# Optimization experiments

Measured on AMD Instinct MI355X. Metric: run time of the kernel, lower is better.

Reference implementation:

```python
import jax, jax.numpy as jnp
import numpy as np
from jax import lax

NEG = -10000.0


def setup_inputs() -> dict:
    key = jax.random.key(0)
    ks = jax.random.split(key, 16)
    T, V, E, H, NT = 2048, 50000, 512, 512, 48  # H = per-direction hidden (hidden_dim//2)
    start, end = NT - 2, NT - 1

    def rn(k, shape, scale=0.05):
        return jax.random.normal(k, shape, jnp.float32) * scale

    words = jax.random.randint(ks[0], (T,), 0, V)
    embed = rn(ks[1], (V, E), 0.1)
    Wih_f = rn(ks[2], (4 * H, E)); Whh_f = rn(ks[3], (4 * H, H))
    bih_f = rn(ks[4], (4 * H,));   bhh_f = rn(ks[5], (4 * H,))
    Wih_b = rn(ks[6], (4 * H, E)); Whh_b = rn(ks[7], (4 * H, H))
    bih_b = rn(ks[8], (4 * H,));   bhh_b = rn(ks[9], (4 * H,))
    W_out = rn(ks[10], (NT, 2 * H)); b_out = rn(ks[11], (NT,))
    transitions = jax.random.normal(ks[12], (NT, NT), jnp.float32)
    # match __init__: no transition into START, none out of END
    transitions = transitions.at[start, :].set(NEG).at[:, end].set(NEG)
    h0 = rn(ks[13], (2, H), 1.0)  # [fwd, bwd] initial hidden (torch.randn in init_hidden)
    c0 = rn(ks[14], (2, H), 1.0)
    return dict(words=words, embed=embed,
                Wih_f=Wih_f, Whh_f=Whh_f, bih_f=bih_f, bhh_f=bhh_f,
                Wih_b=Wih_b, Whh_b=Whh_b, bih_b=bih_b, bhh_b=bhh_b,
                W_out=W_out, b_out=b_out, transitions=transitions,
                h0=h0, c0=c0, start_tag=start, end_tag=end)


def _lstm_dir(x, h0, c0, Wih, Whh, bih, bhh, reverse):
    # x: [T, E]. Precompute input contribution for all steps (one big GEMM).
    xW = x @ Wih.T + (bih + bhh)  # [T, 4H]

    def step(carry, g_in):
        h, c = carry
        g = g_in + h @ Whh.T  # [4H]
        i, f, gg, o = jnp.split(g, 4)
        i = jax.nn.sigmoid(i); f = jax.nn.sigmoid(f)
        gg = jnp.tanh(gg);     o = jax.nn.sigmoid(o)
        c = f * c + i * gg
        h = o * jnp.tanh(c)
        return (h, c), h

    _, hs = lax.scan(step, (h0, c0), xW, reverse=reverse)
    return hs  # [T, H], aligned with input time order


def reference(words, embed, Wih_f, Whh_f, bih_f, bhh_f,
              Wih_b, Whh_b, bih_b, bhh_b,
              W_out, b_out, transitions, h0, c0, start_tag, end_tag):
    x = embed[words]  # [T, E]
    hf = _lstm_dir(x, h0[0], c0[0], Wih_f, Whh_f, bih_f, bhh_f, reverse=False)
    hb = _lstm_dir(x, h0[1], c0[1], Wih_b, Whh_b, bih_b, bhh_b, reverse=True)
    frames = jnp.concatenate([hf, hb], axis=-1) @ W_out.T + b_out  # [T, NT] emissions

    nt = transitions.shape[0]
    tT = transitions.T  # tT[from, to]
    alpha0 = jnp.full((nt,), NEG, frames.dtype).at[start_tag].set(0.0)

    def vstep(alpha, frame):
        # smat[i, j] = alpha[i] + frame[j] + transitions[j, i]
        smat = alpha[:, None] + frame[None, :] + tT
        return smat.max(axis=0), jnp.argmax(smat, axis=0)

    alpha, backtrace = lax.scan(vstep, alpha0, frames)  # backtrace: [T, NT]
    final = alpha + transitions[end_tag]
    best_last = jnp.argmax(final)
    score = final[best_last]

    def back(tag, bp):
        prev = bp[tag]
        return prev, prev

    _, path_head = lax.scan(back, best_last, backtrace[1:], reverse=True)  # [T-1]
    best_path = jnp.concatenate([path_head, best_last[None]])  # [T]
    return score, best_path
```

## Files before the change

kernel.cpp:

```cpp
#include <hip/hip_runtime.h>

#define TT 2048
#define HH 512
#define EE 512
#define NTAGS 48
#define G4 2048
#define NWG 16
#define CANARY 1.0e30f

#define OFF_XW    0ULL
#define OFF_HCAT  (OFF_XW   + 2ULL*TT*G4*4ULL)
#define OFF_FRM   (OFF_HCAT + (unsigned long long)TT*1024ULL*4ULL)
#define OFF_HBUF  (OFF_FRM  + (unsigned long long)TT*NTAGS*4ULL)
#define OFF_BP    (OFF_HBUF + 2ULL*4ULL*HH*4ULL)

__global__ __launch_bounds__(256) void k_xw(
    const int* __restrict__ words, const float* __restrict__ embed,
    const float* __restrict__ WihF, const float* __restrict__ WihB,
    const float* __restrict__ bihF, const float* __restrict__ bhhF,
    const float* __restrict__ bihB, const float* __restrict__ bhhB,
    float* __restrict__ xw, float* __restrict__ hbuf)
{
    const int tid = threadIdx.x;
    const int bx = blockIdx.x, by = blockIdx.y, dir = blockIdx.z;

    if (bx == 0 && by == 0) {
        for (int j = tid; j < 4*HH; j += 256)
            hbuf[dir*4*HH + j] = CANARY;
    }

    const float* Wih = dir ? WihB : WihF;
    const float* bi  = dir ? bihB : bihF;
    const float* bh  = dir ? bhhB : bhhF;

    __shared__ float sa[32][64];
    __shared__ float sb[32][64];
    __shared__ int   wds[64];
    if (tid < 64) wds[tid] = words[by*64 + tid];
    const int tx = tid & 15, ty = tid >> 4;
    float acc[4][4] = {};
    __syncthreads();

    for (int k0 = 0; k0 < EE; k0 += 32) {
        #pragma unroll
        for (int u = 0; u < 2; u++) {
            int idx = tid*2 + u;
            int row = idx >> 3, kq = idx & 7;
            float4 av = *(const float4*)&embed[(size_t)wds[row]*EE + k0 + kq*4];
            float4 bv = *(const float4*)&Wih[(size_t)(bx*64 + row)*EE + k0 + kq*4];
            sa[kq*4+0][row] = av.x; sa[kq*4+1][row] = av.y;
            sa[kq*4+2][row] = av.z; sa[kq*4+3][row] = av.w;
            sb[kq*4+0][row] = bv.x; sb[kq*4+1][row] = bv.y;
            sb[kq*4+2][row] = bv.z; sb[kq*4+3][row] = bv.w;
        }
        __syncthreads();
        #pragma unroll
        for (int k = 0; k < 32; k++) {
            float4 a = *(const float4*)&sa[k][ty*4];
            float4 b = *(const float4*)&sb[k][tx*4];
            acc[0][0] += a.x*b.x; acc[0][1] += a.x*b.y; acc[0][2] += a.x*b.z; acc[0][3] += a.x*b.w;
            acc[1][0] += a.y*b.x; acc[1][1] += a.y*b.y; acc[1][2] += a.y*b.z; acc[1][3] += a.y*b.w;
            acc[2][0] += a.z*b.x; acc[2][1] += a.z*b.y; acc[2][2] += a.z*b.z; acc[2][3] += a.z*b.w;
            acc[3][0] += a.w*b.x; acc[3][1] += a.w*b.y; acc[3][2] += a.w*b.z; acc[3][3] += a.w*b.w;
        }
        __syncthreads();
    }

    float* outp = xw + (size_t)dir*TT*G4;
    const int rbase = bx*64 + tx*4;
    float4 bi4 = *(const float4*)&bi[rbase];
    float4 bh4 = *(const float4*)&bh[rbase];
    float4 bias = make_float4(bi4.x+bh4.x, bi4.y+bh4.y, bi4.z+bh4.z, bi4.w+bh4.w);
    #pragma unroll
    for (int i = 0; i < 4; i++) {
        int t = by*64 + ty*4 + i;
        float4 v = make_float4(acc[i][0]+bias.x, acc[i][1]+bias.y,
                               acc[i][2]+bias.z, acc[i][3]+bias.w);
        *(float4*)&outp[(size_t)t*G4 + rbase] = v;
    }
}

__global__ __launch_bounds__(512, 2) void k_lstm(
    const float* __restrict__ WhhF, const float* __restrict__ WhhB,
    const float* __restrict__ h0, const float* __restrict__ c0,
    const float* __restrict__ xw,
    float* __restrict__ hbuf, float* __restrict__ hcat)
{
    const int bid = blockIdx.x;
    const int dir = bid >> 4;
    const int w   = bid & 15;
    const float* Whh = dir ? WhhB : WhhF;
    const float* xwD = xw + (size_t)dir*TT*G4;
    float* hb = hbuf + dir*4*HH;

    const int tid  = threadIdx.x;
    const int v    = tid >> 6;
    const int l    = tid & 63;
    const int hi   = l >> 4;
    const int gate = (l >> 2) & 3;
    const int q    = l & 3;
    const int hidx = w*32 + v*4 + hi;
    const int row  = gate*HH + hidx;
    const int lb   = l & ~15;

    float4 wreg[32];
    {
        const float4* wr = (const float4*)&Whh[(size_t)row*HH + q*128];
        #pragma unroll
        for (int k = 0; k < 32; k++) wreg[k] = wr[k];
        #pragma unroll
        for (int k = 0; k < 32; k++)
            asm volatile("" : "+v"(wreg[k].x), "+v"(wreg[k].y),
                              "+v"(wreg[k].z), "+v"(wreg[k].w));
    }
    float c = c0[dir*HH + hidx];

    __shared__ __align__(16) float hsh[2][2064];

    {
        float hv = h0[dir*HH + tid];
        #pragma unroll
        for (int r = 0; r < 4; r++) hsh[0][r*516 + tid] = hv;
    }
    __syncthreads();

    float xv = xwD[(size_t)(dir ? TT-1 : 0)*G4 + row];

    for (int s = 0; s < TT; s++) {
        const float* hq = &hsh[s & 1][q*644];
        float p0=0.f,p1=0.f,p2=0.f,p3=0.f;
        #pragma unroll
        for (int k = 0; k < 32; k++) {
            float4 hv = *(const float4*)&hq[4*k];
            p0 += wreg[k].x*hv.x; p1 += wreg[k].y*hv.y;
            p2 += wreg[k].z*hv.z; p3 += wreg[k].w*hv.w;
        }
        float part = (p0+p1)+(p2+p3);
        part += __shfl_xor(part, 1);
        part += __shfl_xor(part, 2);
        if (q == 0) part += xv;

        float gi = __shfl(part, lb);
        float gf = __shfl(part, lb + 4);
        float gg = __shfl(part, lb + 8);
        float go = __shfl(part, lb + 12);

        float i_ = 1.f/(1.f + __expf(-gi) * 0.f + expf(-gi));
        i_ = 1.f/(1.f + expf(-gi));
        float f_ = 1.f/(1.f + expf(-gf));
        float g_ = tanhf(gg);
        float o_ = 1.f/(1.f + expf(-go));
        c = f_*c + i_*g_;
        float hn = o_*tanhf(c);

        const int time = dir ? (TT-1-s) : s;
        if ((l & 15) == 0) {
            hcat[(size_t)time*1024 + dir*HH + hidx] = hn;
            if (s+1 < TT) {
                __hip_atomic_store(&hb[((s+1)&3)*HH + hidx], hn,
                                   __ATOMIC_RELAXED, __HIP_MEMORY_SCOPE_AGENT);
                __hip_atomic_store(&hb[((s+3)&3)*HH + hidx], CANARY,
                                   __ATOMIC_RELAXED, __HIP_MEMORY_SCOPE_AGENT);
            }
        }

        if (s+1 < TT) {
            asm volatile("s_waitcnt vmcnt(0)" ::: "memory");

            xv = xwD[(size_t)(dir ? TT-2-s : s+1)*G4 + row];

            const float* addr = &hb[((s+1)&3)*HH + tid];
            float hv;
            for (;;) {
                hv = __hip_atomic_load(addr, __ATOMIC_RELAXED,
                                       __HIP_MEMORY_SCOPE_AGENT);
                if (hv != CANARY) break;
                __builtin_amdgcn_s_sleep(2);
            }
            #pragma unroll
            for (int r = 0; r < 4; r++) hsh[(s+1)&1][r*516 + tid] = hv;
            __syncthreads();
        }
    }
}

__global__ __launch_bounds__(64) void k_frames(
    const float* __restrict__ hcat, const float* __restrict__ Wout,
    const float* __restrict__ bout, float* __restrict__ frames)
{
    const int t = blockIdx.x, tid = threadIdx.x;
    __shared__ float hrow[1024];
    const float4* src  = (const float4*)&hcat[(size_t)t*1024];
    float4* dst4 = (float4*)hrow;
    #pragma unroll
    for (int u = 0; u < 4; u++) dst4[u*64 + tid] = src[u*64 + tid];
    __syncthreads();
    if (tid < NTAGS) {
        float acc = bout[tid];
        const float4* wr = (const float4*)&Wout[(size_t)tid*1024];
        #pragma unroll 16
        for (int e = 0; e < 256; e++) {
            float4 wv = wr[e];
            float4 hv = dst4[e];
            acc += wv.x*hv.x + wv.y*hv.y + wv.z*hv.z + wv.w*hv.w;
        }
        frames[t*NTAGS + tid] = acc;
    }
}

#define CH 256
__global__ __launch_bounds__(256) void k_viterbi(
    const float* __restrict__ frames, const float* __restrict__ trans,
    const int* __restrict__ startp, const int* __restrict__ endp,
    unsigned char* __restrict__ bp, float* __restrict__ out)
{
    const int tid = threadIdx.x;
    const int grp = tid / NTAGS;
    const int j   = tid % NTAGS;
    __shared__ float alpha[2][NTAGS];
    __shared__ float red[4][NTAGS];
    __shared__ int   redarg[4][NTAGS];
    __shared__ float frbuf[2][NTAGS];
    __shared__ __align__(16) unsigned char bps[CH*NTAGS];
    __shared__ int s_tag;

    float tr[12];
    if (grp < 4) {
        #pragma unroll
        for (int u = 0; u < 12; u++) tr[u] = trans[j*NTAGS + grp*12 + u];
    }
    const int start_tag = *startp;
    if (tid < NTAGS) alpha[0][tid] = (tid == start_tag) ? 0.f : -10000.f;
    const bool is_pf = (tid >= 192 && tid < 192 + NTAGS);
    if (is_pf) frbuf[0][tid-192] = frames[tid-192];
    __syncthreads();

    for (int t = 0; t < TT; t++) {
        float fpre = 0.f;
        if (is_pf && t+1 < TT) fpre = frames[(t+1)*NTAGS + (tid-192)];
        if (grp < 4) {
            float best = -3.0e38f; int barg = 0;
            #pragma unroll
            for (int u = 0; u < 12; u++) {
                float sv = alpha[t&1][grp*12+u] + tr[u];
                if (sv > best) { best = sv; barg = grp*12+u; }
            }
            red[grp][j] = best; redarg[grp][j] = barg;
        }
        __syncthreads();
        if (tid < NTAGS) {
            float b = red[0][tid]; int a = redarg[0][tid];
            #pragma unroll
            for (int g2 = 1; g2 < 4; g2++) {
                float v = red[g2][tid];
                if (v > b) { b = v; a = redarg[g2][tid]; }
            }
            bp[t*NTAGS + tid] = (unsigned char)a;
            alpha[(t+1)&1][tid] = b + frbuf[t&1][tid];
        }
        __syncthreads();
        if (is_pf && t+1 < TT) frbuf[(t+1)&1][tid-192] = fpre;
    }

    if (tid == 0) {
        const int end_tag = *endp;
        float best = -3.0e38f; int bl = 0;
        for (int j2 = 0; j2 < NTAGS; j2++) {
            float v = alpha[0][j2] + trans[end_tag*NTAGS + j2];
            if (v > best) { best = v; bl = j2; }
        }
        out[0] = best;
        out[1 + TT - 1] = (float)bl;
        s_tag = bl;
    }
    __syncthreads();

    for (int base = TT - CH; base >= 0; base -= CH) {
        {
            const float4* srcr = (const float4*)&bp[(size_t)(base + tid)*NTAGS];
            float4* dstr = (float4*)&bps[tid*NTAGS];
            dstr[0] = srcr[0]; dstr[1] = srcr[1]; dstr[2] = srcr[2];
        }
        __syncthreads();
        if (tid == 0) {
            int tag = s_tag;
            const int thi = base + CH - 1;
            const int tlo = (base == 0) ? 1 : base;
            for (int t = thi; t >= tlo; t--) {
                tag = bps[(t - base)*NTAGS + tag];
                out[t] = (float)tag;
            }
            s_tag = tag;
        }
        __syncthreads();
    }
}

extern "C" void kernel_launch(void* const* d_in, const int* in_sizes, int n_in,
                              void* d_out, int out_size, void* d_ws, size_t ws_size,
                              hipStream_t stream)
{
    const int*   words = (const int*)  d_in[0];
    const float* embed = (const float*)d_in[1];
    const float* WihF  = (const float*)d_in[2];
    const float* WhhF  = (const float*)d_in[3];
    const float* bihF  = (const float*)d_in[4];
    const float* bhhF  = (const float*)d_in[5];
    const float* WihB  = (const float*)d_in[6];
    const float* WhhB  = (const float*)d_in[7];
    const float* bihB  = (const float*)d_in[8];
    const float* bhhB  = (const float*)d_in[9];
    const float* Wout  = (const float*)d_in[10];
    const float* bout  = (const float*)d_in[11];
    const float* trans = (const float*)d_in[12];
    const float* h0    = (const float*)d_in[13];
    const float* c0    = (const float*)d_in[14];
    const int*   startp= (const int*)  d_in[15];
    const int*   endp  = (const int*)  d_in[16];

    char* ws = (char*)d_ws;
    float* xw   = (float*)(ws + OFF_XW);
    float* hcat = (float*)(ws + OFF_HCAT);
    float* frm  = (float*)(ws + OFF_FRM);
    float* hbuf = (float*)(ws + OFF_HBUF);
    unsigned char* bp = (unsigned char*)(ws + OFF_BP);

    dim3 g1(32, 32, 2);
    k_xw<<<g1, 256, 0, stream>>>(words, embed, WihF, WihB, bihF, bhhF,
                                 bihB, bhhB, xw, hbuf);
    k_lstm<<<dim3(2*NWG), 512, 0, stream>>>(WhhF, WhhB, h0, c0, xw, hbuf, hcat);
    k_frames<<<dim3(TT), 64, 0, stream>>>(hcat, Wout, bout, frm);
    k_viterbi<<<dim3(1), 256, 0, stream>>>(frm, trans, startp, endp, bp, (float*)d_out);
}
```

Measured before the change: 5.253 ms.

## Restructure LSTM recurrent matvec to split K across 16 lanes per hidden unit

Each lane now holds weights for all four gates over a 32-element slice of the hidden vector and reduces across 16 lanes with xor shuffles. Previously each lane handled one gate row over a quarter of K. The shared hidden buffer shrinks from four replicated padded copies to one padded copy. The store lane no longer polls, so a neighbouring lane loads its element, and the spin loops drop sleep and gain an iteration guard. The aim is cheaper LDS traffic and a shorter critical path per timestep, at the cost of more shuffle rounds. The guard can silently break out early and let stale canary values through.

```diff
diff --git a/kernel.cpp b/kernel.cpp
--- a/kernel.cpp
+++ b/kernel.cpp
@@ -97,88 +97,114 @@
     const int v    = tid >> 6;
     const int l    = tid & 63;
     const int hi   = l >> 4;
-    const int gate = (l >> 2) & 3;
-    const int q    = l & 3;
+    const int k16  = l & 15;
     const int hidx = w*32 + v*4 + hi;
-    const int row  = gate*HH + hidx;
-    const int lb   = l & ~15;
-
-    float4 wreg[32];
-    {
-        const float4* wr = (const float4*)&Whh[(size_t)row*HH + q*128];
-        #pragma unroll
-        for (int k = 0; k < 32; k++) wreg[k] = wr[k];
-        #pragma unroll
-        for (int k = 0; k < 32; k++)
-            asm volatile("" : "+v"(wreg[k].x), "+v"(wreg[k].y),
-                              "+v"(wreg[k].z), "+v"(wreg[k].w));
-    }
+
+    float4 wreg[4][8];
+    #pragma unroll
+    for (int g = 0; g < 4; g++) {
+        const float4* wr = (const float4*)&Whh[(size_t)(g*HH + hidx)*HH + k16*32];
+        #pragma unroll
+        for (int t = 0; t < 8; t++) wreg[g][t] = wr[t];
+    }
+    #pragma unroll
+    for (int g = 0; g < 4; g++)
+        #pragma unroll
+        for (int t = 0; t < 8; t++)
+            asm volatile("" : "+v"(wreg[g][t].x), "+v"(wreg[g][t].y),
+                              "+v"(wreg[g][t].z), "+v"(wreg[g][t].w));
+
     float c = c0[dir*HH + hidx];
 
-    __shared__ __align__(16) float hsh[2][2064];
-
-    {
-        float hv = h0[dir*HH + tid];
-        #pragma unroll
-        for (int r = 0; r < 4; r++) hsh[0][r*516 + tid] = hv;
-    }
-    __syncthreads();
-
-    float xv = xwD[(size_t)(dir ? TT-1 : 0)*G4 + row];
+    __shared__ __align__(16) float hsh[2][16*36];
+
+    hsh[0][(tid>>5)*36 + (tid&31)] = h0[dir*HH + tid];
+    __syncthreads();
+
+    float xv = 0.f;
+    if (k16 < 4) xv = xwD[(size_t)(dir ? TT-1 : 0)*G4 + k16*HH + hidx];
 
     for (int s = 0; s < TT; s++) {
-        const float* hq = &hsh[s & 1][q*644];
-        float p0=0.f,p1=0.f,p2=0.f,p3=0.f;
-        #pragma unroll
-        for (int k = 0; k < 32; k++) {
-            float4 hv = *(const float4*)&hq[4*k];
-            p0 += wreg[k].x*hv.x; p1 += wreg[k].y*hv.y;
-            p2 += wreg[k].z*hv.z; p3 += wreg[k].w*hv.w;
-        }
-        float part = (p0+p1)+(p2+p3);
-        part += __shfl_xor(part, 1);
-        part += __shfl_xor(part, 2);
-        if (q == 0) part += xv;
-
-        float gi = __shfl(part, lb);
-        float gf = __shfl(part, lb + 4);
-        float gg = __shfl(part, lb + 8);
-        float go = __shfl(part, lb + 12);
-
-        float i_ = 1.f/(1.f + __expf(-gi) * 0.f + expf(-gi));
-        i_ = 1.f/(1.f + expf(-gi));
-        float f_ = 1.f/(1.f + expf(-gf));
-        float g_ = tanhf(gg);
-        float o_ = 1.f/(1.f + expf(-go));
-        c = f_*c + i_*g_;
-        float hn = o_*tanhf(c);
+        const float* hc = &hsh[s & 1][k16*36];
+        float4 p = make_float4(0.f, 0.f, 0.f, 0.f);
+        #pragma unroll
+        for (int t = 0; t < 8; t++) {
+            float4 hv = *(const float4*)&hc[4*t];
+            p.x += wreg[0][t].x*hv.x; p.x += wreg[0][t].y*hv.y;
+            p.x += wreg[0][t].z*hv.z; p.x += wreg[0][t].w*hv.w;
+            p.y += wreg[1][t].x*hv.x; p.y += wreg[1][t].y*hv.y;
+            p.y += wreg[1][t].z*hv.z; p.y += wreg[1][t].w*hv.w;
+            p.z += wreg[2][t].x*hv.x; p.z += wreg[2][t].y*hv.y;
+            p.z += wreg[2][t].z*hv.z; p.z += wreg[2][t].w*hv.w;
+            p.w += wreg[3][t].x*hv.x; p.w += wreg[3][t].y*hv.y;
+            p.w += wreg[3][t].z*hv.z; p.w += wreg[3][t].w*hv.w;
+        }
+        if (k16 == 0) p.x += xv;
+        else if (k16 == 1) p.y += xv;
+        else if (k16 == 2) p.z += xv;
+        else if (k16 == 3) p.w += xv;
+
+        #pragma unroll
+        for (int m = 1; m < 16; m <<= 1) {
+            p.x += __shfl_xor(p.x, m);
+            p.y += __shfl_xor(p.y, m);
+            p.z += __shfl_xor(p.z, m);
+            p.w += __shfl_xor(p.w, m);
+        }
+
+        float act = 0.f;
+        if (k16 < 4) {
+            float sv = (k16 == 0) ? p.x : (k16 == 1) ? p.y : (k16 == 2) ? p.z : p.w;
+            act = (k16 == 2) ? tanhf(sv) : 1.f/(1.f + expf(-sv));
+        }
+        const int base = l & ~15;
+        float ai = __shfl(act, base + 0);
+        float af = __shfl(act, base + 1);
+        float ag = __shfl(act, base + 2);
+        float ao = __shfl(act, base + 3);
+        c = af*c + ai*ag;
+        float hn = ao*tanhf(c);
 
         const int time = dir ? (TT-1-s) : s;
-        if ((l & 15) == 0) {
-            hcat[(size_t)time*1024 + dir*HH + hidx] = hn;
+        if (k16 == 4) {
+            asm volatile("s_waitcnt vmcnt(0)" ::: "memory");
             if (s+1 < TT) {
                 __hip_atomic_store(&hb[((s+1)&3)*HH + hidx], hn,
                                    __ATOMIC_RELAXED, __HIP_MEMORY_SCOPE_AGENT);
                 __hip_atomic_store(&hb[((s+3)&3)*HH + hidx], CANARY,
                                    __ATOMIC_RELAXED, __HIP_MEMORY_SCOPE_AGENT);
             }
+            hcat[(size_t)time*1024 + dir*HH + hidx] = hn;
         }
 
         if (s+1 < TT) {
-            asm volatile("s_waitcnt vmcnt(0)" ::: "memory");
-
-            xv = xwD[(size_t)(dir ? TT-2-s : s+1)*G4 + row];
-
-            const float* addr = &hb[((s+1)&3)*HH + tid];
-            float hv;
-            for (;;) {
-                hv = __hip_atomic_load(addr, __ATOMIC_RELAXED,
-                                       __HIP_MEMORY_SCOPE_AGENT);
-                if (hv != CANARY) break;
-                __builtin_amdgcn_s_sleep(2);
-            }
-            #pragma unroll
-            for (int r = 0; r < 4; r++) hsh[(s+1)&1][r*516 + tid] = hv;
+            if (k16 < 4)
+                xv = xwD[(size_t)(dir ? TT-2-s : s+1)*G4 + k16*HH + hidx];
+
+            const int slot = (s+1) & 3;
+            float* dst = &hsh[(s+1) & 1][0];
+            if (k16 == 5) {
+                const float* a0 = &hb[slot*HH + tid];
+                const float* a1 = &hb[slot*HH + tid - 1];
+                float h0v, h1v; int guard = 0;
+                for (;;) {
+                    h0v = __hip_atomic_load(a0, __ATOMIC_RELAXED, __HIP_MEMORY_SCOPE_AGENT);
+                    h1v = __hip_atomic_load(a1, __ATOMIC_RELAXED, __HIP_MEMORY_SCOPE_AGENT);
+                    if (h0v != CANARY && h1v != CANARY) break;
+                    if (++guard > (1<<15)) break;
+                }
+                dst[(tid>>5)*36 + (tid&31)]       = h0v;
+                dst[((tid-1)>>5)*36 + ((tid-1)&31)] = h1v;
+            } else if (k16 != 4) {
+                const float* a0 = &hb[slot*HH + tid];
+                float h0v; int guard = 0;
+                for (;;) {
+                    h0v = __hip_atomic_load(a0, __ATOMIC_RELAXED, __HIP_MEMORY_SCOPE_AGENT);
+                    if (h0v != CANARY) break;
+                    if (++guard > (1<<15)) break;
+                }
+                dst[(tid>>5)*36 + (tid&31)] = h0v;
+            }
             __syncthreads();
         }
     }
```

Measured after the change: 6.515 ms. +24.0%, slower.

## Interleave forward and backward LSTM directions in each workgroup

Applied to the files above, without the earlier changes.

Each of the 32 workgroups now owns 16 hidden units of both directions instead of 32 units of one direction. It keeps both directions' Whh slices in registers, each split 8-way along K with a 3-level shuffle reduction. The forward step's h publish can overlap the backward step's compute, and only half the threads poll global memory, using vectorised dwordx4 loads with sc0/sc1 cache bypass and packed 2-float stores. The polling loop gains a bounded-retry guard that could silently read stale data if a producer stalls.

```diff
diff --git a/kernel.cpp b/kernel.cpp
--- a/kernel.cpp
+++ b/kernel.cpp
@@ -5,8 +5,10 @@
 #define EE 512
 #define NTAGS 48
 #define G4 2048
-#define NWG 16
 #define CANARY 1.0e30f
+
+typedef float f4 __attribute__((ext_vector_type(4)));
+typedef float f2 __attribute__((ext_vector_type(2)));
 
 #define OFF_XW    0ULL
 #define OFF_HCAT  (OFF_XW   + 2ULL*TT*G4*4ULL)
@@ -82,103 +84,162 @@
 
 __global__ __launch_bounds__(512, 2) void k_lstm(
     const float* __restrict__ WhhF, const float* __restrict__ WhhB,
-    const float* __restrict__ h0, const float* __restrict__ c0,
+    const float* __restrict__ h0, const float* __restrict__ cinit,
     const float* __restrict__ xw,
     float* __restrict__ hbuf, float* __restrict__ hcat)
 {
-    const int bid = blockIdx.x;
-    const int dir = bid >> 4;
-    const int w   = bid & 15;
-    const float* Whh = dir ? WhhB : WhhF;
-    const float* xwD = xw + (size_t)dir*TT*G4;
-    float* hb = hbuf + dir*4*HH;
-
-    const int tid  = threadIdx.x;
-    const int v    = tid >> 6;
-    const int l    = tid & 63;
-    const int hi   = l >> 4;
-    const int gate = (l >> 2) & 3;
-    const int q    = l & 3;
-    const int hidx = w*32 + v*4 + hi;
-    const int row  = gate*HH + hidx;
-    const int lb   = l & ~15;
-
-    float4 wreg[32];
+    const int w   = blockIdx.x;
+    const int tid = threadIdx.x;
+    const int v   = tid >> 6;
+    const int l   = tid & 63;
+    const int o   = l >> 5;
+    const int g   = (l >> 3) & 3;
+    const int k8  = l & 7;
+    const int hidx = w*16 + v*2 + o;
+    const int row  = g*HH + hidx;
+
+    float* hb0 = hbuf;
+    float* hb1 = hbuf + 4*HH;
+    const float* xw0 = xw;
+    const float* xw1 = xw + (size_t)TT*G4;
+
+    float4 w0[16], w1[16];
     {
-        const float4* wr = (const float4*)&Whh[(size_t)row*HH + q*128];
-        #pragma unroll
-        for (int k = 0; k < 32; k++) wreg[k] = wr[k];
-        #pragma unroll
-        for (int k = 0; k < 32; k++)
-            asm volatile("" : "+v"(wreg[k].x), "+v"(wreg[k].y),
-                              "+v"(wreg[k].z), "+v"(wreg[k].w));
-    }
-    float c = c0[dir*HH + hidx];
-
-    __shared__ __align__(16) float hsh[2][2064];
-
+        const float4* p0 = (const float4*)&WhhF[(size_t)row*HH + k8*64];
+        const float4* p1 = (const float4*)&WhhB[(size_t)row*HH + k8*64];
+        #pragma unroll
+        for (int t = 0; t < 16; t++) { w0[t] = p0[t]; w1[t] = p1[t]; }
+        #pragma unroll
+        for (int t = 0; t < 16; t++) {
+            asm volatile("" : "+v"(w0[t].x), "+v"(w0[t].y), "+v"(w0[t].z), "+v"(w0[t].w));
+            asm volatile("" : "+v"(w1[t].x), "+v"(w1[t].y), "+v"(w1[t].z), "+v"(w1[t].w));
+        }
+    }
+    float c0r = cinit[0*HH + hidx];
+    float c1r = cinit[1*HH + hidx];
+
+    __shared__ __align__(16) float hsh[2][2][8*68];
     {
-        float hv = h0[dir*HH + tid];
-        #pragma unroll
-        for (int r = 0; r < 4; r++) hsh[0][r*516 + tid] = hv;
-    }
-    __syncthreads();
-
-    float xv = xwD[(size_t)(dir ? TT-1 : 0)*G4 + row];
+        int ch = tid >> 6, of = tid & 63;
+        hsh[0][0][ch*68 + of] = h0[0*HH + tid];
+        hsh[0][1][ch*68 + of] = h0[1*HH + tid];
+    }
+    __syncthreads();
+
+    float xv0 = 0.f, xv1 = 0.f;
+    if (k8 == 0) {
+        xv0 = xw0[(size_t)0*G4 + row];
+        xv1 = xw1[(size_t)(TT-1)*G4 + row];
+    }
+
+    const int ob = l & 32;
 
     for (int s = 0; s < TT; s++) {
-        const float* hq = &hsh[s & 1][q*644];
-        float p0=0.f,p1=0.f,p2=0.f,p3=0.f;
-        #pragma unroll
-        for (int k = 0; k < 32; k++) {
-            float4 hv = *(const float4*)&hq[4*k];
-            p0 += wreg[k].x*hv.x; p1 += wreg[k].y*hv.y;
-            p2 += wreg[k].z*hv.z; p3 += wreg[k].w*hv.w;
-        }
-        float part = (p0+p1)+(p2+p3);
-        part += __shfl_xor(part, 1);
-        part += __shfl_xor(part, 2);
-        if (q == 0) part += xv;
-
-        float gi = __shfl(part, lb);
-        float gf = __shfl(part, lb + 4);
-        float gg = __shfl(part, lb + 8);
-        float go = __shfl(part, lb + 12);
-
-        float i_ = 1.f/(1.f + __expf(-gi) * 0.f + expf(-gi));
-        i_ = 1.f/(1.f + expf(-gi));
-        float f_ = 1.f/(1.f + expf(-gf));
-        float g_ = tanhf(gg);
-        float o_ = 1.f/(1.f + expf(-go));
-        c = f_*c + i_*g_;
-        float hn = o_*tanhf(c);
-
-        const int time = dir ? (TT-1-s) : s;
-        if ((l & 15) == 0) {
-            hcat[(size_t)time*1024 + dir*HH + hidx] = hn;
-            if (s+1 < TT) {
-                __hip_atomic_store(&hb[((s+1)&3)*HH + hidx], hn,
-                                   __ATOMIC_RELAXED, __HIP_MEMORY_SCOPE_AGENT);
-                __hip_atomic_store(&hb[((s+3)&3)*HH + hidx], CANARY,
-                                   __ATOMIC_RELAXED, __HIP_MEMORY_SCOPE_AGENT);
+        float h0n;
+        {
+            const float* hc = &hsh[s & 1][0][k8*68];
+            float p0=0.f,p1=0.f,p2=0.f,p3=0.f;
+            #pragma unroll
+            for (int t = 0; t < 16; t++) {
+                float4 hv = *(const float4*)&hc[4*t];
+                p0 += w0[t].x*hv.x; p1 += w0[t].y*hv.y;
+                p2 += w0[t].z*hv.z; p3 += w0[t].w*hv.w;
+            }
+            float p = (p0+p1)+(p2+p3);
+            if (k8 == 0) p += xv0;
+            p += __shfl_xor(p, 1); p += __shfl_xor(p, 2); p += __shfl_xor(p, 4);
+            float gi = __shfl(p, ob+0),  gf = __shfl(p, ob+8);
+            float gg = __shfl(p, ob+16), go = __shfl(p, ob+24);
+            float i_ = 1.f/(1.f + expf(-gi));
+            float f_ = 1.f/(1.f + expf(-gf));
+            float g_ = tanhf(gg);
+            float o_ = 1.f/(1.f + expf(-go));
+            c0r = f_*c0r + i_*g_;
+            h0n = o_*tanhf(c0r);
+        }
+        {
+            float ha = __shfl(h0n, 0), hbv = __shfl(h0n, 32);
+            if (l == 0) {
+                f2 pack = {ha, hbv};
+                const int b2 = w*16 + v*2;
+                asm volatile("s_waitcnt vmcnt(0)" ::: "memory");
+                if (s+1 < TT) {
+                    const float* ah = &hb0[((s+1)&3)*HH + b2];
+                    const float* ac = &hb0[((s+3)&3)*HH + b2];
+                    f2 can = {CANARY, CANARY};
+                    asm volatile("global_store_dwordx2 %0, %1, off sc0 sc1"
+                                 :: "v"(ah), "v"(pack) : "memory");
+                    asm volatile("global_store_dwordx2 %0, %1, off sc0 sc1"
+                                 :: "v"(ac), "v"(can) : "memory");
+                }
+                *(f2*)&hcat[(size_t)s*1024 + 0*HH + b2] = pack;
+            }
+        }
+
+        float h1n;
+        {
+            const float* hc = &hsh[s & 1][1][k8*68];
+            float p0=0.f,p1=0.f,p2=0.f,p3=0.f;
+            #pragma unroll
+            for (int t = 0; t < 16; t++) {
+                float4 hv = *(const float4*)&hc[4*t];
+                p0 += w1[t].x*hv.x; p1 += w1[t].y*hv.y;
+                p2 += w1[t].z*hv.z; p3 += w1[t].w*hv.w;
+            }
+            float p = (p0+p1)+(p2+p3);
+            if (k8 == 0) p += xv1;
+            p += __shfl_xor(p, 1); p += __shfl_xor(p, 2); p += __shfl_xor(p, 4);
+            float gi = __shfl(p, ob+0),  gf = __shfl(p, ob+8);
+            float gg = __shfl(p, ob+16), go = __shfl(p, ob+24);
+            float i_ = 1.f/(1.f + expf(-gi));
+            float f_ = 1.f/(1.f + expf(-gf));
+            float g_ = tanhf(gg);
+            float o_ = 1.f/(1.f + expf(-go));
+            c1r = f_*c1r + i_*g_;
+            h1n = o_*tanhf(c1r);
+        }
+        {
+            float ha = __shfl(h1n, 0), hbv = __shfl(h1n, 32);
+            if (l == 0) {
+                f2 pack = {ha, hbv};
+                const int b2 = w*16 + v*2;
+                if (s+1 < TT) {
+                    const float* ah = &hb1[((s+1)&3)*HH + b2];
+                    const float* ac = &hb1[((s+3)&3)*HH + b2];
+                    f2 can = {CANARY, CANARY};
+                    asm volatile("global_store_dwordx2 %0, %1, off sc0 sc1"
+                                 :: "v"(ah), "v"(pack) : "memory");
+                    asm volatile("global_store_dwordx2 %0, %1, off sc0 sc1"
+                                 :: "v"(ac), "v"(can) : "memory");
+                }
+                *(f2*)&hcat[(size_t)(TT-1-s)*1024 + 1*HH + b2] = pack;
             }
         }
 
         if (s+1 < TT) {
-            asm volatile("s_waitcnt vmcnt(0)" ::: "memory");
-
-            xv = xwD[(size_t)(dir ? TT-2-s : s+1)*G4 + row];
-
-            const float* addr = &hb[((s+1)&3)*HH + tid];
-            float hv;
-            for (;;) {
-                hv = __hip_atomic_load(addr, __ATOMIC_RELAXED,
-                                       __HIP_MEMORY_SCOPE_AGENT);
-                if (hv != CANARY) break;
-                __builtin_amdgcn_s_sleep(2);
-            }
-            #pragma unroll
-            for (int r = 0; r < 4; r++) hsh[(s+1)&1][r*516 + tid] = hv;
+            if (k8 == 0) {
+                xv0 = xw0[(size_t)(s+1)*G4 + row];
+                xv1 = xw1[(size_t)(TT-2-s)*G4 + row];
+            }
+
+            const int slot = (s+1) & 3;
+            if (v < 4) {
+                const int d   = v >> 1;
+                const int pv  = v & 1;
+                const int fbase = (pv*64 + l)*4;
+                const float* ap = (d ? hb1 : hb0) + slot*HH + fbase;
+                f4 hv; int guard = 0;
+                for (;;) {
+                    asm volatile("global_load_dwordx4 %0, %1, off sc0 sc1\n\t"
+                                 "s_waitcnt vmcnt(0)"
+                                 : "=v"(hv) : "v"(ap) : "memory");
+                    if (hv.x != CANARY && hv.y != CANARY &&
+                        hv.z != CANARY && hv.w != CANARY) break;
+                    if (++guard > (1<<17)) break;
+                    __builtin_amdgcn_s_sleep(1);
+                }
+                *(f4*)&hsh[(s+1)&1][d][(fbase>>6)*68 + (fbase&63)] = hv;
+            }
             __syncthreads();
         }
     }
@@ -328,7 +389,7 @@
     dim3 g1(32, 32, 2);
     k_xw<<<g1, 256, 0, stream>>>(words, embed, WihF, WihB, bihF, bhhF,
                                  bihB, bhhB, xw, hbuf);
-    k_lstm<<<dim3(2*NWG), 512, 0, stream>>>(WhhF, WhhB, h0, c0, xw, hbuf, hcat);
+    k_lstm<<<dim3(32), 512, 0, stream>>>(WhhF, WhhB, h0, c0, xw, hbuf, hcat);
     k_frames<<<dim3(TT), 64, 0, stream>>>(hcat, Wout, bout, frm);
     k_viterbi<<<dim3(1), 256, 0, stream>>>(frm, trans, startp, endp, bp, (float*)d_out);
 }
```

New measurement: 8.666 ms. +65.0%, slower.
